# Kernel optimization log

Hardware: AMD Instinct MI355X
Metric: run time of the kernel (lower is better)

## Reference

```python
import jax, jax.numpy as jnp
import numpy as np

NC, M, D = 4, 512, 64
COMMITMENT_COST = 0.25


def setup_inputs() -> dict:
    key = jax.random.key(0)
    k1, k2 = jax.random.split(key)
    N = 65536
    x = jax.random.normal(k1, (N, NC * D), dtype=jnp.float32)
    # original init: uniform(-1/m, 1/m); randn*small keeps comparable scale
    embedding = jax.random.normal(k2, (NC, M, D), dtype=jnp.float32) * (1.0 / M)
    mask = jnp.ones((N, NC), dtype=jnp.float32)
    return {"x": x, "embedding": embedding, "mask": mask}


def reference(x, embedding, mask):
    nc, m, d = embedding.shape
    x_flat = x.reshape(-1, nc, d)                      # (N, nc, d)
    xd = jax.lax.stop_gradient(x_flat)                 # detached copy

    # squared-distance search expressed as a GEMM (same math as sum((x-e)^2)):
    x2 = jnp.sum(xd * xd, axis=-1)[:, :, None]
    e2 = jnp.sum(embedding * embedding, axis=-1)[None, :, :]
    xe = jnp.einsum('ncd,cmd->ncm', xd, embedding)
    distances = x2 - 2.0 * xe + e2

    indices = jnp.argmin(distances, axis=-1)           # (N, nc) int
    # gather nearest code vectors: (N, nc, d)
    quantized = embedding[jnp.arange(nc)[None, :], indices]
    quantized = quantized * mask[..., None]

    codebook_loss = jnp.mean((jax.lax.stop_gradient(x_flat) - quantized) ** 2)
    e_latent_loss = jnp.mean((x_flat - jax.lax.stop_gradient(quantized)) ** 2)
    commitment_loss = COMMITMENT_COST * e_latent_loss

    # straight-through estimator
    quantized_st = x_flat + jax.lax.stop_gradient(quantized - x_flat)
    quantized_st = quantized_st.reshape(x.shape)

    # perplexity via per-codebook histogram (avoids N x nc x m one-hot)
    counts = jax.vmap(lambda idx: jnp.bincount(idx, length=m))(indices.T)  # (nc, m)
    avg_probs = counts.astype(x.dtype) / x_flat.shape[0]
    perplexity = jnp.exp(-jnp.sum(avg_probs * jnp.log(avg_probs + 1e-10)))

    return (quantized_st, commitment_loss, codebook_loss, perplexity, indices)
```

## Files before the change

### kernel.cpp

```cpp
#include <hip/hip_runtime.h>
#include <math.h>
#include <float.h>

#define NTOK 65536
#define NCB  4
#define MCODE 512
#define DIM  64

#define QST_SIZE (NTOK * NCB * DIM)
#define IDX_OFF  (QST_SIZE + 3)

#define TOK_TILE  128

#define WS_EH 0
#define WS_EL 262144
#define WS_D0 524288
#define WS_CNT 532480
#define WS_LOSS 540672

typedef _Float16 half8 __attribute__((ext_vector_type(8)));
typedef float floatx16 __attribute__((ext_vector_type(16)));

__global__ __launch_bounds__(256) void prep_kernel(const float* __restrict__ emb,
                                                   _Float16* __restrict__ ehf,
                                                   _Float16* __restrict__ elf,
                                                   float* __restrict__ d0p,
                                                   int* __restrict__ counts,
                                                   float* __restrict__ lossSum) {
    int row = blockIdx.x * 256 + threadIdx.x;
    if (row >= NCB * MCODE) return;
    const int c   = row >> 9;
    const int n   = row & 511;
    const int nt  = n >> 5;
    const int r5  = n & 31;
    const float* src = emb + (size_t)row * DIM;

    float s = 0.f;
#pragma unroll
    for (int ch = 0; ch < 4; ++ch) {
#pragma unroll
        for (int h = 0; h < 2; ++h) {
            half8 hv, lv;
#pragma unroll
            for (int t = 0; t < 8; ++t) {
                float e = src[ch * 16 + h * 8 + t];
                s += e * e;
                float f = e * 512.0f;
                _Float16 hi = (_Float16)f;
                float r = f - (float)hi;
                hv[t] = hi;
                lv[t] = (_Float16)r;
            }
            size_t off = ((size_t)((c * 16 + nt) * 4 + ch)) * 512 + (h * 32 + r5) * 8;
            *(half8*)(ehf + off) = hv;
            *(half8*)(elf + off) = lv;
        }
    }
    d0p[row] = -256.0f * s;
    counts[row] = 0;
    if (row == 0) *lossSum = 0.f;
}

__global__ __launch_bounds__(256) void vq_main(const float* __restrict__ x,
                                               const float* __restrict__ emb,
                                               const float* __restrict__ mask,
                                               const _Float16* __restrict__ ehf,
                                               const _Float16* __restrict__ elf,
                                               const float* __restrict__ d0p,
                                               int* __restrict__ counts,
                                               float* __restrict__ lossSum,
                                               float* __restrict__ outQ,
                                               float* __restrict__ outIdx) {
    __shared__ __align__(16) _Float16 As[2][4096];
    __shared__ __align__(16) float d0s[MCODE];
    __shared__ int   Is[TOK_TILE];
    __shared__ float wls[4];

    const int tid  = threadIdx.x;
    const int c    = blockIdx.y;
    const int n0tk = blockIdx.x * TOK_TILE;
    const int lane = tid & 63;
    const int w    = tid >> 6;
    const int l31  = lane & 31;
    const int hi   = lane >> 5;
    const int hi4  = hi * 4;

    const _Float16* gEh = ehf + (size_t)c * (16 * 4 * 512);
    const _Float16* gEl = elf + (size_t)c * (16 * 4 * 512);

    float4 sh = *(const float4*)(gEh + tid * 8);
    float4 sl = *(const float4*)(gEl + tid * 8);
    float4 dstage;
    if (tid < 128) dstage = *(const float4*)(d0p + c * MCODE + tid * 4);

    half8 Bh[4], Bl[4];
    {
        const float* xr = x + (size_t)(n0tk + w * 32 + l31) * (NCB * DIM) + c * DIM + hi * 8;
#pragma unroll
        for (int ch = 0; ch < 4; ++ch) {
            float fv[8];
            *(float4*)(fv)     = *(const float4*)(xr + ch * 16);
            *(float4*)(fv + 4) = *(const float4*)(xr + ch * 16 + 4);
            half8 h8, l8;
#pragma unroll
            for (int t = 0; t < 8; ++t) {
                float f = fv[t];
                _Float16 hh = (_Float16)f;
                h8[t] = hh;
                l8[t] = (_Float16)(f - (float)hh);
            }
            Bh[ch] = h8;
            Bl[ch] = l8;
        }
    }

    *(float4*)((char*)&As[0][0]    + tid * 16) = sh;
    *(float4*)((char*)&As[0][2048] + tid * 16) = sl;
    if (tid < 128) *(float4*)(&d0s[tid * 4]) = dstage;
    __syncthreads();

    float maxv = -FLT_MAX;
    int   maxn = 0;

    for (int nt = 0; nt < 16; ++nt) {
        const int p = nt & 1;

        float4 nh, nl;
        if (nt < 15) {
            nh = *(const float4*)(gEh + (nt + 1) * 2048 + tid * 8);
            nl = *(const float4*)(gEl + (nt + 1) * 2048 + tid * 8);
        }

        const _Float16* ah = &As[p][0] + lane * 8;
        const _Float16* al = &As[p][2048] + lane * 8;
        half8 Ah0 = *(const half8*)(ah);
        half8 Ah1 = *(const half8*)(ah + 512);
        half8 Ah2 = *(const half8*)(ah + 1024);
        half8 Ah3 = *(const half8*)(ah + 1536);
        half8 Al0 = *(const half8*)(al);
        half8 Al1 = *(const half8*)(al + 512);
        half8 Al2 = *(const half8*)(al + 1024);
        half8 Al3 = *(const half8*)(al + 1536);

        const float* dpt = &d0s[nt * 32 + hi4];
        float4 d40 = *(const float4*)(dpt);
        float4 d41 = *(const float4*)(dpt + 8);
        float4 d42 = *(const float4*)(dpt + 16);
        float4 d43 = *(const float4*)(dpt + 24);
        floatx16 acc;
        acc[0]  = d40.x; acc[1]  = d40.y; acc[2]  = d40.z; acc[3]  = d40.w;
        acc[4]  = d41.x; acc[5]  = d41.y; acc[6]  = d41.z; acc[7]  = d41.w;
        acc[8]  = d42.x; acc[9]  = d42.y; acc[10] = d42.z; acc[11] = d42.w;
        acc[12] = d43.x; acc[13] = d43.y; acc[14] = d43.z; acc[15] = d43.w;

        acc = __builtin_amdgcn_mfma_f32_32x32x16_f16(Ah0, Bh[0], acc, 0, 0, 0);
        acc = __builtin_amdgcn_mfma_f32_32x32x16_f16(Al0, Bh[0], acc, 0, 0, 0);
        acc = __builtin_amdgcn_mfma_f32_32x32x16_f16(Ah0, Bl[0], acc, 0, 0, 0);
        acc = __builtin_amdgcn_mfma_f32_32x32x16_f16(Ah1, Bh[1], acc, 0, 0, 0);
        acc = __builtin_amdgcn_mfma_f32_32x32x16_f16(Al1, Bh[1], acc, 0, 0, 0);
        acc = __builtin_amdgcn_mfma_f32_32x32x16_f16(Ah1, Bl[1], acc, 0, 0, 0);
        acc = __builtin_amdgcn_mfma_f32_32x32x16_f16(Ah2, Bh[2], acc, 0, 0, 0);
        acc = __builtin_amdgcn_mfma_f32_32x32x16_f16(Al2, Bh[2], acc, 0, 0, 0);
        acc = __builtin_amdgcn_mfma_f32_32x32x16_f16(Ah2, Bl[2], acc, 0, 0, 0);
        acc = __builtin_amdgcn_mfma_f32_32x32x16_f16(Ah3, Bh[3], acc, 0, 0, 0);
        acc = __builtin_amdgcn_mfma_f32_32x32x16_f16(Al3, Bh[3], acc, 0, 0, 0);
        acc = __builtin_amdgcn_mfma_f32_32x32x16_f16(Ah3, Bl[3], acc, 0, 0, 0);

        const int nbase = nt * 32 + hi4;
#pragma unroll
        for (int r = 0; r < 16; ++r) {
            float m = acc[r];
            int   n = nbase + ((r & 3) + 8 * (r >> 2));
            if (m > maxv) { maxv = m; maxn = n; }
        }

        if (nt < 15) {
            *(float4*)((char*)&As[p ^ 1][0]    + tid * 16) = nh;
            *(float4*)((char*)&As[p ^ 1][2048] + tid * 16) = nl;
        }
        __syncthreads();
    }

    {
        float ov = __shfl_xor(maxv, 32);
        int   on = __shfl_xor(maxn, 32);
        if (ov > maxv || (ov == maxv && on < maxn)) { maxv = ov; maxn = on; }
    }

    if (hi == 0) {
        Is[w * 32 + l31] = maxn;
        atomicAdd(&counts[c * MCODE + maxn], 1);
        outIdx[(size_t)(n0tk + w * 32 + l31) * NCB + c] = (float)maxn;
    }
    __syncthreads();

    float lloss = 0.f;
#pragma unroll
    for (int i = 0; i < 8; ++i) {
        int q = tid + i * 256;
        int tok = q >> 4, d4 = q & 15;
        int idx = Is[tok];
        float mv = mask[(size_t)(n0tk + tok) * NCB + c];
        float4 e4 = *(const float4*)(emb + ((size_t)c * MCODE + idx) * DIM + d4 * 4);
        float4 x4 = *(const float4*)(x + (size_t)(n0tk + tok) * (NCB * DIM) + c * DIM + d4 * 4);
        float qx = e4.x * mv, qy = e4.y * mv, qz = e4.z * mv, qw = e4.w * mv;
        float4 o;
        o.x = x4.x + (qx - x4.x);
        o.y = x4.y + (qy - x4.y);
        o.z = x4.z + (qz - x4.z);
        o.w = x4.w + (qw - x4.w);
        *(float4*)(outQ + (size_t)(n0tk + tok) * (NCB * DIM) + c * DIM + d4 * 4) = o;
        float dx = x4.x - qx, dy = x4.y - qy, dz = x4.z - qz, dw = x4.w - qw;
        lloss += dx * dx + dy * dy + dz * dz + dw * dw;
    }
#pragma unroll
    for (int off = 32; off > 0; off >>= 1) lloss += __shfl_xor(lloss, off);
    if ((tid & 63) == 0) wls[tid >> 6] = lloss;
    __syncthreads();
    if (tid == 0) {
        float s = wls[0] + wls[1] + wls[2] + wls[3];
        atomicAdd(lossSum, s);
    }
}

__global__ __launch_bounds__(256) void finalize_kernel(const int* __restrict__ counts,
                                                       const float* __restrict__ lossSum,
                                                       float* __restrict__ out) {
    __shared__ float wls[4];
    int tid = threadIdx.x;
    float s = 0.f;
#pragma unroll
    for (int i = 0; i < 8; ++i) {
        int j = tid + i * 256;
        float p = (float)counts[j] * (1.0f / 65536.0f);
        s += p * logf(p + 1e-10f);
    }
#pragma unroll
    for (int off = 32; off > 0; off >>= 1) s += __shfl_xor(s, off);
    if ((tid & 63) == 0) wls[tid >> 6] = s;
    __syncthreads();
    if (tid == 0) {
        float tot = wls[0] + wls[1] + wls[2] + wls[3];
        float L = *lossSum * (1.0f / (float)QST_SIZE);
        out[QST_SIZE + 0] = 0.25f * L;
        out[QST_SIZE + 1] = L;
        out[QST_SIZE + 2] = expf(-tot);
    }
}

extern "C" void kernel_launch(void* const* d_in, const int* in_sizes, int n_in,
                              void* d_out, int out_size, void* d_ws, size_t ws_size,
                              hipStream_t stream) {
    const float* x    = (const float*)d_in[0];
    const float* emb  = (const float*)d_in[1];
    const float* mask = (const float*)d_in[2];
    float* out = (float*)d_out;

    _Float16* ehf  = (_Float16*)((char*)d_ws + WS_EH);
    _Float16* elf  = (_Float16*)((char*)d_ws + WS_EL);
    float* d0p     = (float*)((char*)d_ws + WS_D0);
    int*   counts  = (int*)((char*)d_ws + WS_CNT);
    float* lossSum = (float*)((char*)d_ws + WS_LOSS);

    prep_kernel<<<dim3(8), dim3(256), 0, stream>>>(emb, ehf, elf, d0p, counts, lossSum);
    vq_main<<<dim3(NTOK / TOK_TILE, NCB), dim3(256), 0, stream>>>(
        x, emb, mask, ehf, elf, d0p, counts, lossSum, out, out + IDX_OFF);
    finalize_kernel<<<dim3(1), dim3(256), 0, stream>>>(counts, lossSum, out);
}
```

Baseline: 202.6 us.

## Process two code tiles per barrier with split MFMA accumulator chains

The codebook loop now stages two 32-code tiles per shared-memory buffer, which halves the number of barrier-separated iterations. The 12-MFMA dependency chain is split into two interleaved accumulators, and the running argmax is kept in four independent groups to shorten serial compare chains. Launch bounds also request 3 blocks per CU. The cost is twice the LDS footprint, more registers, and a slightly different floating-point summation order that could change near-tie argmin results.

```diff
diff --git a/kernel.cpp b/kernel.cpp
--- a/kernel.cpp
+++ b/kernel.cpp
@@ -61,17 +61,17 @@
     if (row == 0) *lossSum = 0.f;
 }
 
-__global__ __launch_bounds__(256) void vq_main(const float* __restrict__ x,
-                                               const float* __restrict__ emb,
-                                               const float* __restrict__ mask,
-                                               const _Float16* __restrict__ ehf,
-                                               const _Float16* __restrict__ elf,
-                                               const float* __restrict__ d0p,
-                                               int* __restrict__ counts,
-                                               float* __restrict__ lossSum,
-                                               float* __restrict__ outQ,
-                                               float* __restrict__ outIdx) {
-    __shared__ __align__(16) _Float16 As[2][4096];
+__global__ __launch_bounds__(256, 3) void vq_main(const float* __restrict__ x,
+                                                  const float* __restrict__ emb,
+                                                  const float* __restrict__ mask,
+                                                  const _Float16* __restrict__ ehf,
+                                                  const _Float16* __restrict__ elf,
+                                                  const float* __restrict__ d0p,
+                                                  int* __restrict__ counts,
+                                                  float* __restrict__ lossSum,
+                                                  float* __restrict__ outQ,
+                                                  float* __restrict__ outIdx) {
+    __shared__ __align__(16) _Float16 As[2][8192];
     __shared__ __align__(16) float d0s[MCODE];
     __shared__ int   Is[TOK_TILE];
     __shared__ float wls[4];
@@ -88,8 +88,10 @@
     const _Float16* gEh = ehf + (size_t)c * (16 * 4 * 512);
     const _Float16* gEl = elf + (size_t)c * (16 * 4 * 512);
 
-    float4 sh = *(const float4*)(gEh + tid * 8);
-    float4 sl = *(const float4*)(gEl + tid * 8);
+    float4 sh0 = *(const float4*)(gEh + tid * 8);
+    float4 sl0 = *(const float4*)(gEl + tid * 8);
+    float4 sh1 = *(const float4*)(gEh + 2048 + tid * 8);
+    float4 sl1 = *(const float4*)(gEl + 2048 + tid * 8);
     float4 dstage;
     if (tid < 128) dstage = *(const float4*)(d0p + c * MCODE + tid * 4);
 
@@ -114,71 +116,98 @@
         }
     }
 
-    *(float4*)((char*)&As[0][0]    + tid * 16) = sh;
-    *(float4*)((char*)&As[0][2048] + tid * 16) = sl;
+    *(float4*)((char*)&As[0][0]           + tid * 16) = sh0;
+    *(float4*)((char*)&As[0][2048]        + tid * 16) = sl0;
+    *(float4*)((char*)&As[0][4096]        + tid * 16) = sh1;
+    *(float4*)((char*)&As[0][4096 + 2048] + tid * 16) = sl1;
     if (tid < 128) *(float4*)(&d0s[tid * 4]) = dstage;
     __syncthreads();
 
-    float maxv = -FLT_MAX;
-    int   maxn = 0;
-
-    for (int nt = 0; nt < 16; ++nt) {
-        const int p = nt & 1;
-
-        float4 nh, nl;
-        if (nt < 15) {
-            nh = *(const float4*)(gEh + (nt + 1) * 2048 + tid * 8);
-            nl = *(const float4*)(gEl + (nt + 1) * 2048 + tid * 8);
-        }
-
-        const _Float16* ah = &As[p][0] + lane * 8;
-        const _Float16* al = &As[p][2048] + lane * 8;
-        half8 Ah0 = *(const half8*)(ah);
-        half8 Ah1 = *(const half8*)(ah + 512);
-        half8 Ah2 = *(const half8*)(ah + 1024);
-        half8 Ah3 = *(const half8*)(ah + 1536);
-        half8 Al0 = *(const half8*)(al);
-        half8 Al1 = *(const half8*)(al + 512);
-        half8 Al2 = *(const half8*)(al + 1024);
-        half8 Al3 = *(const half8*)(al + 1536);
-
-        const float* dpt = &d0s[nt * 32 + hi4];
-        float4 d40 = *(const float4*)(dpt);
-        float4 d41 = *(const float4*)(dpt + 8);
-        float4 d42 = *(const float4*)(dpt + 16);
-        float4 d43 = *(const float4*)(dpt + 24);
-        floatx16 acc;
-        acc[0]  = d40.x; acc[1]  = d40.y; acc[2]  = d40.z; acc[3]  = d40.w;
-        acc[4]  = d41.x; acc[5]  = d41.y; acc[6]  = d41.z; acc[7]  = d41.w;
-        acc[8]  = d42.x; acc[9]  = d42.y; acc[10] = d42.z; acc[11] = d42.w;
-        acc[12] = d43.x; acc[13] = d43.y; acc[14] = d43.z; acc[15] = d43.w;
-
-        acc = __builtin_amdgcn_mfma_f32_32x32x16_f16(Ah0, Bh[0], acc, 0, 0, 0);
-        acc = __builtin_amdgcn_mfma_f32_32x32x16_f16(Al0, Bh[0], acc, 0, 0, 0);
-        acc = __builtin_amdgcn_mfma_f32_32x32x16_f16(Ah0, Bl[0], acc, 0, 0, 0);
-        acc = __builtin_amdgcn_mfma_f32_32x32x16_f16(Ah1, Bh[1], acc, 0, 0, 0);
-        acc = __builtin_amdgcn_mfma_f32_32x32x16_f16(Al1, Bh[1], acc, 0, 0, 0);
-        acc = __builtin_amdgcn_mfma_f32_32x32x16_f16(Ah1, Bl[1], acc, 0, 0, 0);
-        acc = __builtin_amdgcn_mfma_f32_32x32x16_f16(Ah2, Bh[2], acc, 0, 0, 0);
-        acc = __builtin_amdgcn_mfma_f32_32x32x16_f16(Al2, Bh[2], acc, 0, 0, 0);
-        acc = __builtin_amdgcn_mfma_f32_32x32x16_f16(Ah2, Bl[2], acc, 0, 0, 0);
-        acc = __builtin_amdgcn_mfma_f32_32x32x16_f16(Ah3, Bh[3], acc, 0, 0, 0);
-        acc = __builtin_amdgcn_mfma_f32_32x32x16_f16(Al3, Bh[3], acc, 0, 0, 0);
-        acc = __builtin_amdgcn_mfma_f32_32x32x16_f16(Ah3, Bl[3], acc, 0, 0, 0);
-
-        const int nbase = nt * 32 + hi4;
-#pragma unroll
-        for (int r = 0; r < 16; ++r) {
-            float m = acc[r];
-            int   n = nbase + ((r & 3) + 8 * (r >> 2));
-            if (m > maxv) { maxv = m; maxn = n; }
-        }
-
-        if (nt < 15) {
-            *(float4*)((char*)&As[p ^ 1][0]    + tid * 16) = nh;
-            *(float4*)((char*)&As[p ^ 1][2048] + tid * 16) = nl;
+    float gv[4];
+    int   gn[4];
+#pragma unroll
+    for (int g = 0; g < 4; ++g) { gv[g] = -FLT_MAX; gn[g] = 0; }
+
+    for (int j = 0; j < 8; ++j) {
+        const int b = j & 1;
+
+        float4 nh0, nl0, nh1, nl1;
+        if (j < 7) {
+            const int base = (2 * j + 2) * 2048;
+            nh0 = *(const float4*)(gEh + base + tid * 8);
+            nl0 = *(const float4*)(gEl + base + tid * 8);
+            nh1 = *(const float4*)(gEh + base + 2048 + tid * 8);
+            nl1 = *(const float4*)(gEl + base + 2048 + tid * 8);
+        }
+
+#pragma unroll
+        for (int slot = 0; slot < 2; ++slot) {
+            const int nt = 2 * j + slot;
+
+            const _Float16* ah = &As[b][slot * 4096] + lane * 8;
+            const _Float16* al = ah + 2048;
+            half8 Ah0 = *(const half8*)(ah);
+            half8 Ah1 = *(const half8*)(ah + 512);
+            half8 Ah2 = *(const half8*)(ah + 1024);
+            half8 Ah3 = *(const half8*)(ah + 1536);
+            half8 Al0 = *(const half8*)(al);
+            half8 Al1 = *(const half8*)(al + 512);
+            half8 Al2 = *(const half8*)(al + 1024);
+            half8 Al3 = *(const half8*)(al + 1536);
+
+            const float* dpt = &d0s[nt * 32 + hi4];
+            float4 d40 = *(const float4*)(dpt);
+            float4 d41 = *(const float4*)(dpt + 8);
+            float4 d42 = *(const float4*)(dpt + 16);
+            float4 d43 = *(const float4*)(dpt + 24);
+            floatx16 acc0, acc1;
+            acc0[0]  = d40.x; acc0[1]  = d40.y; acc0[2]  = d40.z; acc0[3]  = d40.w;
+            acc0[4]  = d41.x; acc0[5]  = d41.y; acc0[6]  = d41.z; acc0[7]  = d41.w;
+            acc0[8]  = d42.x; acc0[9]  = d42.y; acc0[10] = d42.z; acc0[11] = d42.w;
+            acc0[12] = d43.x; acc0[13] = d43.y; acc0[14] = d43.z; acc0[15] = d43.w;
+#pragma unroll
+            for (int r = 0; r < 16; ++r) acc1[r] = 0.f;
+
+            acc1 = __builtin_amdgcn_mfma_f32_32x32x16_f16(Ah2, Bh[2], acc1, 0, 0, 0);
+            acc0 = __builtin_amdgcn_mfma_f32_32x32x16_f16(Ah0, Bh[0], acc0, 0, 0, 0);
+            acc1 = __builtin_amdgcn_mfma_f32_32x32x16_f16(Al2, Bh[2], acc1, 0, 0, 0);
+            acc0 = __builtin_amdgcn_mfma_f32_32x32x16_f16(Al0, Bh[0], acc0, 0, 0, 0);
+            acc1 = __builtin_amdgcn_mfma_f32_32x32x16_f16(Ah2, Bl[2], acc1, 0, 0, 0);
+            acc0 = __builtin_amdgcn_mfma_f32_32x32x16_f16(Ah0, Bl[0], acc0, 0, 0, 0);
+            acc1 = __builtin_amdgcn_mfma_f32_32x32x16_f16(Ah3, Bh[3], acc1, 0, 0, 0);
+            acc0 = __builtin_amdgcn_mfma_f32_32x32x16_f16(Ah1, Bh[1], acc0, 0, 0, 0);
+            acc1 = __builtin_amdgcn_mfma_f32_32x32x16_f16(Al3, Bh[3], acc1, 0, 0, 0);
+            acc0 = __builtin_amdgcn_mfma_f32_32x32x16_f16(Al1, Bh[1], acc0, 0, 0, 0);
+            acc1 = __builtin_amdgcn_mfma_f32_32x32x16_f16(Ah3, Bl[3], acc1, 0, 0, 0);
+            acc0 = __builtin_amdgcn_mfma_f32_32x32x16_f16(Ah1, Bl[1], acc0, 0, 0, 0);
+
+            const int nbase = nt * 32 + hi4;
+#pragma unroll
+            for (int g = 0; g < 4; ++g) {
+#pragma unroll
+                for (int q = 0; q < 4; ++q) {
+                    const int r = g * 4 + q;
+                    float m = acc0[r] + acc1[r];
+                    int   n = nbase + 8 * g + q;
+                    if (m > gv[g]) { gv[g] = m; gn[g] = n; }
+                }
+            }
+        }
+
+        if (j < 7) {
+            *(float4*)((char*)&As[b ^ 1][0]           + tid * 16) = nh0;
+            *(float4*)((char*)&As[b ^ 1][2048]        + tid * 16) = nl0;
+            *(float4*)((char*)&As[b ^ 1][4096]        + tid * 16) = nh1;
+            *(float4*)((char*)&As[b ^ 1][4096 + 2048] + tid * 16) = nl1;
         }
         __syncthreads();
+    }
+
+    float maxv = gv[0];
+    int   maxn = gn[0];
+#pragma unroll
+    for (int g = 1; g < 4; ++g) {
+        if (gv[g] > maxv || (gv[g] == maxv && gn[g] < maxn)) { maxv = gv[g]; maxn = gn[g]; }
     }
 
     {
```

After: 205.8 us. About the same (+1.6%).
